# Kernel optimization log

Hardware: AMD Instinct MI355X
Metric: run time of the kernel (lower is better)

## Reference

```python
import jax, jax.numpy as jnp
import numpy as np

G = 64        # supervoxel grid per dim (cfg.orig_grid_shape)
CELL = 16     # pixels per grid cell
T = 32        # tile size in px (covers 2x2 cells)
NT = 32       # tiles per dim per shift config
CH = 40       # Conv_trio channels


def setup_inputs() -> dict:
    key = jax.random.key(0)
    ks = jax.random.split(key, 8)
    W = G * CELL
    curr_image = jax.random.normal(ks[0], (W, W), jnp.float32)
    # masks encode per-pixel supervoxel id (pixel belongs to cell floor(px/CELL))
    ids = (jnp.arange(G)[:, None] * G + jnp.arange(G)[None, :]).astype(jnp.float32)
    masks = jnp.repeat(jnp.repeat(ids, CELL, axis=0), CELL, axis=1)[..., None]
    return {
        'curr_image': curr_image,
        'masks': masks,
        'conv1_w': jax.random.normal(ks[1], (3, 3, 1, CH), jnp.float32) * 0.1,
        'conv1_b': jnp.zeros((CH,), jnp.float32),
        'ln1_s': jnp.ones((CH,), jnp.float32),
        'ln1_b': jnp.zeros((CH,), jnp.float32),
        'conv2_w': jax.random.normal(ks[2], (3, 3, CH, CH), jnp.float32) * 0.1,
        'conv2_b': jnp.zeros((CH,), jnp.float32),
        'ln2_s': jnp.ones((CH,), jnp.float32),
        'ln2_b': jnp.zeros((CH,), jnp.float32),
        'dense_w': jax.random.normal(ks[3], ((T // 4) * (T // 4) * CH, 6), jnp.float32) * 0.02,
        'dense_b': jnp.zeros((6,), jnp.float32),
    }


def _tile(a):
    # [W, W, c] -> [NT*NT, T, T, c]
    c = a.shape[-1]
    return a.reshape(NT, T, NT, T, c).transpose(0, 2, 1, 3, 4).reshape(NT * NT, T, T, c)


def _config_tokens(img, masks, ids, sx, sy):
    # shifted tiling: tile (i,j) covers px [T*i + sx*CELL, ...)
    rolled_img = jnp.roll(img, (-sx * CELL, -sy * CELL), (0, 1))
    rolled_msk = jnp.roll(masks, (-sx * CELL, -sy * CELL), (0, 1))
    img_t = _tile(rolled_img)          # [NT*NT, T, T, 1]
    msk_t = _tile(rolled_msk)[..., 0]  # [NT*NT, T, T]
    curr_ids = ids[sx::2, sy::2].reshape(-1)  # [NT*NT]
    filt = (msk_t == curr_ids[:, None, None]).astype(img_t.dtype)
    return img_t * filt[..., None]


def _conv_trio(x, w, b, s, bln):
    y = jax.lax.conv_general_dilated(x, w, (2, 2), 'SAME',
                                     dimension_numbers=('NHWC', 'HWIO', 'NHWC')) + b
    mu = jnp.mean(y, axis=-1, keepdims=True)
    var = jnp.var(y, axis=-1, keepdims=True)
    y = (y - mu) * jax.lax.rsqrt(var + 1e-6) * s + bln
    return jax.nn.gelu(y)


def reference(curr_image, masks, conv1_w, conv1_b, ln1_s, ln1_b,
              conv2_w, conv2_b, ln2_s, ln2_b, dense_w, dense_b):
    img = curr_image[..., None]  # [W, W, 1]
    ids = (jnp.arange(G)[:, None] * G + jnp.arange(G)[None, :]).astype(masks.dtype)
    tokens = jnp.concatenate([
        _config_tokens(img, masks, ids, 0, 0),
        _config_tokens(img, masks, ids, 1, 0),
        _config_tokens(img, masks, ids, 0, 1),
        _config_tokens(img, masks, ids, 1, 1),
    ], axis=0)  # [4*NT*NT, T, T, 1]
    x = _conv_trio(tokens, conv1_w, conv1_b, ln1_s, ln1_b)  # [F, 16, 16, 40]
    x = _conv_trio(x, conv2_w, conv2_b, ln2_s, ln2_b)       # [F, 8, 8, 40]
    x = x.reshape(x.shape[0], -1)
    return x @ dense_w + dense_b  # node embeddings [F, 6]
```

## Files before the change

kernel.cpp:

```cpp
#include <hip/hip_runtime.h>
#include <math.h>

#define CH 40
#define IMW 1024
#define TOKH (9*10*40)
#define W2T_HALVES (48*48*8)
#define Z1_OFF W2T_HALVES
#define OUTC_OFF (Z1_OFF + 40)

typedef _Float16 v8h __attribute__((ext_vector_type(8)));
typedef float    v4f __attribute__((ext_vector_type(4)));
typedef float    v2f __attribute__((ext_vector_type(2)));

__device__ __forceinline__ float gelu_fast(float x) {
    float u = 1.5957691216057308f * (x + 0.044715f * x * x * x);
    return x * __builtin_amdgcn_rcpf(1.0f + __expf(-u));
}

__global__ __launch_bounds__(256) void prep_kernel(
    const float* __restrict__ w2,
    const float* __restrict__ b1, const float* __restrict__ s1,
    const float* __restrict__ bb1,
    const float* __restrict__ b2, const float* __restrict__ s2,
    const float* __restrict__ bb2,
    const float* __restrict__ dw, const float* __restrict__ db,
    _Float16* __restrict__ ws)
{
    const int t = threadIdx.x;
    int idx0 = blockIdx.x * 256 + t;
    for (int idx = idx0; idx < W2T_HALVES; idx += gridDim.x * 256) {
        int j   = idx & 7;
        int co  = (idx >> 3) % 48;
        int kgg = idx / (48 * 8);
        int k   = kgg * 8 + j;
        float v = 0.0f;
        if (co < CH && k < 360) {
            int wi = k / 40, ci = k - wi * 40;
            v = w2[(wi * CH + ci) * CH + co];
        }
        ws[idx] = (_Float16)v;
    }
    if (blockIdx.x != 0) return;

    __shared__ float zs[40];
    __shared__ float w2sum[9][40];
    __shared__ float p2l[120];
    __shared__ float red[4][6];

    if (t < 120) p2l[t] = (t < 40) ? b2[t] : (t < 80 ? s2[t - 40] : bb2[t - 80]);

    if (t >= 64 && t < 128) {
        int lane = t - 64;
        bool act = lane < CH;
        float bv = act ? b1[lane] : 0.f;
        float s = bv;
        #pragma unroll
        for (int m = 1; m < 64; m <<= 1) s += __shfl_xor(s, m, 64);
        float mu = s * (1.0f / CH);
        float d = act ? (bv - mu) : 0.f;
        float q = d * d;
        #pragma unroll
        for (int m = 1; m < 64; m <<= 1) q += __shfl_xor(q, m, 64);
        float rs = rsqrtf(q * (1.0f / CH) + 1e-6f);
        if (act) {
            float g = gelu_fast((bv - mu) * rs * s1[lane] + bb1[lane]);
            zs[lane] = g;
            ws[Z1_OFF + lane] = (_Float16)g;
        }
    }
    __syncthreads();

    for (int idx = t; idx < 360; idx += 256) {
        int wi = idx / 40, ch = idx - wi * 40;
        float s = 0.f;
        #pragma unroll
        for (int ci = 0; ci < CH; ci++)
            s += w2[(wi * CH + ci) * CH + ch] * zs[ci];
        w2sum[wi][ch] = s;
    }
    __syncthreads();

    {
        const int m = t >> 2, sub = t & 3;
        const int p = m >> 3, q = m & 7;
        const int co0 = sub * 10;
        float a6[6] = {0.f, 0.f, 0.f, 0.f, 0.f, 0.f};
        if (p >= 4 || q >= 4) {
            const int drmax = (p == 7) ? 2 : 3;
            const int dcmax = (q == 7) ? 2 : 3;
            float vv[10];
            float s_own = 0.f;
            #pragma unroll
            for (int u = 0; u < 10; u++) {
                float v = p2l[co0 + u];
                for (int dr = 0; dr < drmax; dr++)
                    for (int dc = 0; dc < dcmax; dc++)
                        v += w2sum[dr * 3 + dc][co0 + u];
                vv[u] = v; s_own += v;
            }
            s_own += __shfl_xor(s_own, 1, 64);
            s_own += __shfl_xor(s_own, 2, 64);
            float mu = s_own * (1.0f / CH);
            float v_own = 0.f;
            #pragma unroll
            for (int u = 0; u < 10; u++) { float d = vv[u] - mu; v_own += d * d; }
            v_own += __shfl_xor(v_own, 1, 64);
            v_own += __shfl_xor(v_own, 2, 64);
            float rs = rsqrtf(v_own * (1.0f / CH) + 1e-6f);
            const float* wp = &dw[(m * CH + co0) * 6];
            #pragma unroll
            for (int u = 0; u < 10; u++) {
                float gv = gelu_fast((vv[u] - mu) * rs * p2l[40 + co0 + u] + p2l[80 + co0 + u]);
                v2f w01 = *(const v2f*)&wp[u * 6];
                v2f w23 = *(const v2f*)&wp[u * 6 + 2];
                v2f w45 = *(const v2f*)&wp[u * 6 + 4];
                a6[0] += gv * w01[0]; a6[1] += gv * w01[1];
                a6[2] += gv * w23[0]; a6[3] += gv * w23[1];
                a6[4] += gv * w45[0]; a6[5] += gv * w45[1];
            }
        }
        #pragma unroll
        for (int off = 32; off > 0; off >>= 1)
            #pragma unroll
            for (int k = 0; k < 6; k++) a6[k] += __shfl_down(a6[k], off, 64);
        int wv = t >> 6, lane = t & 63;
        if (lane == 0) {
            #pragma unroll
            for (int k = 0; k < 6; k++) red[wv][k] = a6[k];
        }
        __syncthreads();
        if (t == 0) {
            float* oc = (float*)&ws[OUTC_OFF];
            #pragma unroll
            for (int k = 0; k < 6; k++)
                oc[k] = red[0][k] + red[1][k] + red[2][k] + red[3][k] + db[k];
        }
    }
}

__global__ __launch_bounds__(256) void sgn_kernel(
    const float* __restrict__ img,
    const float* __restrict__ w1, const float* __restrict__ b1,
    const float* __restrict__ s1, const float* __restrict__ bb1,
    const float* __restrict__ b2, const float* __restrict__ s2,
    const float* __restrict__ bb2,
    const float* __restrict__ dw,
    const _Float16* __restrict__ ws,
    float* __restrict__ out)
{
    __shared__ __align__(16) _Float16 x1h[4 * TOKH];
    __shared__ float w1t[40 * 12];
    __shared__ float p1s[120];
    __shared__ float p2s[120];
    __shared__ unsigned koff_s[48];

    const int t    = threadIdx.x;
    const int wv   = t >> 6;
    const int lane = t & 63;

    const int f   = blockIdx.x * 4 + wv;
    const int cfg = f >> 10;
    const int ij  = f & 1023;
    const int ti  = ij >> 5, tj = ij & 31;
    const int cr  = 2 * ti + (cfg & 1);
    const int cc  = 2 * tj + (cfg >> 1);

    float vin[9];
    {
        const int r = lane >> 3, c = lane & 7;
        const float* ib = &img[(cr * 16) * IMW + cc * 16];
        #pragma unroll
        for (int dr = 0; dr < 3; dr++)
            #pragma unroll
            for (int dc = 0; dc < 3; dc++) {
                int rr = 2 * r + dr, cp = 2 * c + dc;
                vin[dr * 3 + dc] = (rr < 16 && cp < 16) ? ib[rr * IMW + cp] : 0.0f;
            }
    }
    const v8h* zsrc = (const v8h*)&ws[Z1_OFF];
    v8h z0 = zsrc[0], z1v = zsrc[1], z2v = zsrc[2], z3v = zsrc[3], z4v = zsrc[4];

    for (int i = t; i < 360; i += 256) {
        int k = i / 40, ch = i - k * 40;
        w1t[ch * 12 + k] = w1[i];
    }
    if (t < 120) {
        p1s[t] = (t < 40) ? b1[t] : (t < 80 ? s1[t - 40] : bb1[t - 80]);
    } else if (t >= 128 && t < 248) {
        int i = t - 128;
        p2s[i] = (i < 40) ? b2[i] : (i < 80 ? s2[i - 40] : bb2[i - 80]);
    }
    if (t < 48) {
        int k0 = 8 * t;
        unsigned v = 0;
        if (k0 < 360) {
            int wi = k0 / 40, ci0 = k0 - wi * 40;
            int dr = wi / 3, dc = wi - 3 * dr;
            v = (unsigned)((dr * 10 + dc) * 40 + ci0);
        }
        koff_s[t] = v;
    }
    __syncthreads();

    _Float16* x1w = &x1h[wv * TOKH];

    {
        const int r = lane >> 3, c = lane & 7;
        float y[40];
        float s = 0.f;
        #pragma unroll
        for (int ch = 0; ch < 40; ch++) {
            float a = p1s[ch];
            const float* wr = &w1t[ch * 12];
            #pragma unroll
            for (int k = 0; k < 9; k++) a += vin[k] * wr[k];
            y[ch] = a; s += a;
        }
        float mu = s * (1.0f / CH);
        float q = 0.f;
        #pragma unroll
        for (int ch = 0; ch < 40; ch++) { float d = y[ch] - mu; q += d * d; }
        float rs = rsqrtf(q * (1.0f / CH) + 1e-6f);
        const int base = (r * 10 + c) * 40;
        #pragma unroll
        for (int chk = 0; chk < 5; chk++) {
            v8h hv;
            #pragma unroll
            for (int jj = 0; jj < 8; jj++) {
                int ch = chk * 8 + jj;
                hv[jj] = (_Float16)gelu_fast((y[ch] - mu) * rs * p1s[40 + ch] + p1s[80 + ch]);
            }
            *(v8h*)&x1w[base + chk * 8] = hv;
        }
    }
    if (lane < 17) {
        int rr = (lane < 9) ? 8 : (lane - 9);
        int cb = (lane < 9) ? lane : 8;
        int base = (rr * 10 + cb) * 40;
        *(v8h*)&x1w[base]      = z0;
        *(v8h*)&x1w[base + 8]  = z1v;
        *(v8h*)&x1w[base + 16] = z2v;
        *(v8h*)&x1w[base + 24] = z3v;
        *(v8h*)&x1w[base + 32] = z4v;
    }
    __builtin_amdgcn_s_waitcnt(0);

    v4f acc0 = {0,0,0,0}, acc1 = {0,0,0,0}, acc2 = {0,0,0,0};
    const int row = lane & 15;
    const int kg  = lane >> 4;
    {
        const unsigned pbase = (unsigned)((20 * (row >> 2) + 2 * (row & 3)) * 40);
        __builtin_amdgcn_s_setprio(1);
        #pragma unroll
        for (int s = 0; s < 12; s++) {
            const int kc = (s << 2) | kg;
            unsigned aoff = pbase + koff_s[kc];
            v8h a = *(const v8h*)&x1w[aoff];
            const _Float16* wb = &ws[(kc * 48 + row) * 8];
            v8h bf0 = *(const v8h*)&wb[0];
            v8h bf1 = *(const v8h*)&wb[16 * 8];
            v8h bf2 = *(const v8h*)&wb[32 * 8];
            acc0 = __builtin_amdgcn_mfma_f32_16x16x32_f16(a, bf0, acc0, 0, 0, 0);
            acc1 = __builtin_amdgcn_mfma_f32_16x16x32_f16(a, bf1, acc1, 0, 0, 0);
            acc2 = __builtin_amdgcn_mfma_f32_16x16x32_f16(a, bf2, acc2, 0, 0, 0);
        }
        __builtin_amdgcn_s_setprio(0);
    }

    {
        const int cix = row;
        const bool h2 = (cix < 8);
        const float b2a = p2s[cix],      b2b = p2s[16 + cix],  b2c = h2 ? p2s[32 + cix] : 0.f;
        const float s2a = p2s[40 + cix], s2b = p2s[56 + cix],  s2c = h2 ? p2s[72 + cix] : 0.f;
        const float g2a = p2s[80 + cix], g2b = p2s[96 + cix],  g2c = h2 ? p2s[112 + cix] : 0.f;
        float a6[6] = {0.f, 0.f, 0.f, 0.f, 0.f, 0.f};
        #pragma unroll
        for (int j = 0; j < 4; j++) {
            const int m = (kg << 2) | j;
            float v0 = acc0[j] + b2a;
            float v1 = acc1[j] + b2b;
            float v2 = h2 ? (acc2[j] + b2c) : 0.f;
            float s = v0 + v1 + v2;
            s += __shfl_xor(s, 1, 64);
            s += __shfl_xor(s, 2, 64);
            s += __shfl_xor(s, 4, 64);
            s += __shfl_xor(s, 8, 64);
            float mu = s * (1.0f / CH);
            float d0 = v0 - mu, d1 = v1 - mu, d2 = v2 - mu;
            float q = d0 * d0 + d1 * d1 + (h2 ? d2 * d2 : 0.f);
            q += __shfl_xor(q, 1, 64);
            q += __shfl_xor(q, 2, 64);
            q += __shfl_xor(q, 4, 64);
            q += __shfl_xor(q, 8, 64);
            float rs = rsqrtf(q * (1.0f / CH) + 1e-6f);
            float g0 = gelu_fast(d0 * rs * s2a + g2a);
            float g1 = gelu_fast(d1 * rs * s2b + g2b);
            float g2 = h2 ? gelu_fast(d2 * rs * s2c + g2c) : 0.f;
            const int drow = ((m >> 2) * 8 + (m & 3)) * CH;
            const float* w0p = &dw[(drow + cix) * 6];
            const float* w1p = &dw[(drow + 16 + cix) * 6];
            const float* w2p = &dw[(drow + 32 + cix) * 6];
            #pragma unroll
            for (int k = 0; k < 6; k++)
                a6[k] += g0 * w0p[k] + g1 * w1p[k] + g2 * w2p[k];
        }
        #pragma unroll
        for (int off = 32; off > 0; off >>= 1)
            #pragma unroll
            for (int k = 0; k < 6; k++) a6[k] += __shfl_down(a6[k], off, 64);
        if (lane == 0) {
            const float* oc = (const float*)&ws[OUTC_OFF];
            #pragma unroll
            for (int k = 0; k < 6; k++) out[f * 6 + k] = a6[k] + oc[k];
        }
    }
}

extern "C" void kernel_launch(void* const* d_in, const int* in_sizes, int n_in,
                              void* d_out, int out_size, void* d_ws, size_t ws_size,
                              hipStream_t stream) {
    const float* img = (const float*)d_in[0];
    const float* w1  = (const float*)d_in[2];
    const float* b1  = (const float*)d_in[3];
    const float* s1  = (const float*)d_in[4];
    const float* bb1 = (const float*)d_in[5];
    const float* w2  = (const float*)d_in[6];
    const float* b2  = (const float*)d_in[7];
    const float* s2  = (const float*)d_in[8];
    const float* bb2 = (const float*)d_in[9];
    const float* dw  = (const float*)d_in[10];
    const float* db  = (const float*)d_in[11];
    float* out = (float*)d_out;
    _Float16* ws = (_Float16*)d_ws;

    prep_kernel<<<32, 256, 0, stream>>>(w2, b1, s1, bb1, b2, s2, bb2, dw, db, ws);
    sgn_kernel<<<1024, 256, 0, stream>>>(img, w1, b1, s1, bb1,
                                         b2, s2, bb2, dw, ws, out);
}
```

Before: 33.33 us.

## Split conv1 channels across lanes with shuffle-reduced LayerNorm

Conv1 work is redistributed so that each lane handles 5 channels across all 8 rows of one column, with those channels' weights held in registers, instead of computing all 40 channels for a single output pixel. LayerNorm mean and variance are reduced across the 8 lanes sharing a pixel using xor shuffles. The aim is to lower register pressure and cut the LDS weight reads repeated per lane. In exchange it adds a serial loop over rows, repeated image loads, shuffle latency, and scalar fp16 LDS stores in place of vector stores.

```diff
diff --git a/kernel.cpp b/kernel.cpp
--- a/kernel.cpp
+++ b/kernel.cpp
@@ -165,18 +165,6 @@
     const int cr  = 2 * ti + (cfg & 1);
     const int cc  = 2 * tj + (cfg >> 1);
 
-    float vin[9];
-    {
-        const int r = lane >> 3, c = lane & 7;
-        const float* ib = &img[(cr * 16) * IMW + cc * 16];
-        #pragma unroll
-        for (int dr = 0; dr < 3; dr++)
-            #pragma unroll
-            for (int dc = 0; dc < 3; dc++) {
-                int rr = 2 * r + dr, cp = 2 * c + dc;
-                vin[dr * 3 + dc] = (rr < 16 && cp < 16) ? ib[rr * IMW + cp] : 0.0f;
-            }
-    }
     const v8h* zsrc = (const v8h*)&ws[Z1_OFF];
     v8h z0 = zsrc[0], z1v = zsrc[1], z2v = zsrc[2], z3v = zsrc[3], z4v = zsrc[4];
 
@@ -205,32 +193,53 @@
     _Float16* x1w = &x1h[wv * TOKH];
 
     {
-        const int r = lane >> 3, c = lane & 7;
-        float y[40];
-        float s = 0.f;
-        #pragma unroll
-        for (int ch = 0; ch < 40; ch++) {
-            float a = p1s[ch];
-            const float* wr = &w1t[ch * 12];
-            #pragma unroll
-            for (int k = 0; k < 9; k++) a += vin[k] * wr[k];
-            y[ch] = a; s += a;
-        }
-        float mu = s * (1.0f / CH);
-        float q = 0.f;
-        #pragma unroll
-        for (int ch = 0; ch < 40; ch++) { float d = y[ch] - mu; q += d * d; }
-        float rs = rsqrtf(q * (1.0f / CH) + 1e-6f);
-        const int base = (r * 10 + c) * 40;
-        #pragma unroll
-        for (int chk = 0; chk < 5; chk++) {
-            v8h hv;
-            #pragma unroll
-            for (int jj = 0; jj < 8; jj++) {
-                int ch = chk * 8 + jj;
-                hv[jj] = (_Float16)gelu_fast((y[ch] - mu) * rs * p1s[40 + ch] + p1s[80 + ch]);
+        const int c   = lane & 7;
+        const int ch0 = (lane >> 3) * 5;
+        float wreg[5][9];
+        float b1v[5], s1v[5], g1v[5];
+        #pragma unroll
+        for (int u = 0; u < 5; u++) {
+            #pragma unroll
+            for (int k = 0; k < 9; k++) wreg[u][k] = w1t[(ch0 + u) * 12 + k];
+            b1v[u] = p1s[ch0 + u];
+            s1v[u] = p1s[40 + ch0 + u];
+            g1v[u] = p1s[80 + ch0 + u];
+        }
+        const float* ib = &img[(cr * 16) * IMW + cc * 16];
+        #pragma unroll 2
+        for (int r = 0; r < 8; r++) {
+            float vin[9];
+            #pragma unroll
+            for (int dr = 0; dr < 3; dr++)
+                #pragma unroll
+                for (int dc = 0; dc < 3; dc++) {
+                    int rr = 2 * r + dr, cp = 2 * c + dc;
+                    vin[dr * 3 + dc] = (rr < 16 && cp < 16) ? ib[rr * IMW + cp] : 0.0f;
+                }
+            float y[5];
+            float s_own = 0.f;
+            #pragma unroll
+            for (int u = 0; u < 5; u++) {
+                float a = b1v[u];
+                #pragma unroll
+                for (int k = 0; k < 9; k++) a += vin[k] * wreg[u][k];
+                y[u] = a; s_own += a;
             }
-            *(v8h*)&x1w[base + chk * 8] = hv;
+            s_own += __shfl_xor(s_own, 8, 64);
+            s_own += __shfl_xor(s_own, 16, 64);
+            s_own += __shfl_xor(s_own, 32, 64);
+            float mu = s_own * (1.0f / CH);
+            float v_own = 0.f;
+            #pragma unroll
+            for (int u = 0; u < 5; u++) { float d = y[u] - mu; v_own += d * d; }
+            v_own += __shfl_xor(v_own, 8, 64);
+            v_own += __shfl_xor(v_own, 16, 64);
+            v_own += __shfl_xor(v_own, 32, 64);
+            float rs = rsqrtf(v_own * (1.0f / CH) + 1e-6f);
+            const int base = (r * 10 + c) * 40 + ch0;
+            #pragma unroll
+            for (int u = 0; u < 5; u++)
+                x1w[base + u] = (_Float16)gelu_fast((y[u] - mu) * rs * s1v[u] + g1v[u]);
         }
     }
     if (lane < 17) {
```

New measurement: 35.14 us. 5.4% more time.
